# Optimization experiments

Hardware: AMD Instinct MI355X
Metric: run time of the kernel (lower is better)

The kernel has to match this reference:

```python
import jax, jax.numpy as jnp
import numpy as np

B, S, D = 4, 2048, 1024

def setup_inputs() -> dict:
    key = jax.random.key(0)
    k1, k2, k3, k4 = jax.random.split(key, 4)
    scale = 1.0 / np.sqrt(D)
    token_encodings = jax.random.normal(k1, (B, S, D), dtype=jnp.float32)
    W_q = jax.random.normal(k2, (D, D), dtype=jnp.float32) * scale
    W_k = jax.random.normal(k3, (D, D), dtype=jnp.float32) * scale
    W_v = jax.random.normal(k4, (D, D), dtype=jnp.float32) * scale
    # causal mask, broadcastable to (B, S, S); 0 means masked
    mask = jnp.tril(jnp.ones((S, S), dtype=jnp.int32))[None, :, :]
    return {"token_encodings": token_encodings, "mask": mask,
            "W_q": W_q, "W_k": W_k, "W_v": W_v}

def reference(token_encodings, mask, W_q, W_k, W_v):
    # nn.Linear(d, d, bias=False): y = x @ W.T
    q = jnp.einsum('bsd,ed->bse', token_encodings, W_q)
    k = jnp.einsum('bsd,ed->bse', token_encodings, W_k)
    v = jnp.einsum('bsd,ed->bse', token_encodings, W_v)
    d_k = q.shape[-1]
    scores = jnp.einsum('bqd,bkd->bqk', q, k) / jnp.sqrt(jnp.asarray(d_k, q.dtype))
    scores = jnp.where(mask == 0, jnp.asarray(-jnp.inf, scores.dtype), scores)
    attn_weights = jax.nn.softmax(scores, axis=-1)
    output = jnp.einsum('bqk,bkd->bqd', attn_weights, v)
    return (output, attn_weights)
```

## Files before the change

### kernel.cpp

```cpp
#include <hip/hip_runtime.h>
#include <hip/hip_bf16.h>
#include <stdint.h>
#include <math.h>


typedef __hip_bfloat16 bf16;
typedef __attribute__((ext_vector_type(8))) short short8;
typedef __attribute__((ext_vector_type(4))) float f32x4;

#define BM 128
#define BN 128
#define BK 64

static constexpr int Bb = 4;
static constexpr int S  = 2048;
static constexpr int D  = 1024;
static constexpr size_t QK_ELEMS = (size_t)Bb * S * D;
static constexpr size_t SS_ELEMS = (size_t)S * S;
static constexpr size_t W_ELEMS  = (size_t)D * D;

__device__ __forceinline__ void async16(const bf16* g, bf16* l) {
  __builtin_amdgcn_global_load_lds(
      (__attribute__((address_space(1))) const void*)g,
      (__attribute__((address_space(3))) void*)l, 16, 0, 0);
}

template<bool SWAP>
__device__ __forceinline__ void gemm_core(const bf16* __restrict__ A,
                                          const bf16* __restrict__ B,
                                          int ldA, int ldB, int ksteps,
                                          bf16* As, bf16* Bs,
                                          f32x4 acc[4][4])
{
  const int tid  = threadIdx.x;
  const int lane = tid & 63;
  const int wave = tid >> 6;
  const int wm   = (wave & 1) * 64;
  const int wn   = (wave >> 1) * 64;
  const int m16  = lane & 15;
  const int kq   = lane >> 4;
  const int sw   = m16 & 7;

  int r[4], f[4];
  #pragma unroll
  for (int i = 0; i < 4; ++i) {
    const int c = tid + i * 256;
    r[i] = c >> 3;
    f[i] = (((c & 7) ^ (r[i] & 7))) * 8;
  }

  for (int ks = 0; ks < ksteps; ++ks) {
    const int k = ks * BK;
    #pragma unroll
    for (int i = 0; i < 4; ++i)
      async16(A + (size_t)r[i] * ldA + k + f[i], As + ((size_t)tid + i * 256) * 8);
    #pragma unroll
    for (int i = 0; i < 4; ++i)
      async16(B + (size_t)r[i] * ldB + k + f[i], Bs + ((size_t)tid + i * 256) * 8);
    __syncthreads();

    #pragma unroll
    for (int j = 0; j < 2; ++j) {
      const int jc = j * 4 + kq;
      const int sl = jc ^ sw;
      short8 af[4], bfr[4];
      #pragma unroll
      for (int i = 0; i < 4; ++i)
        af[i] = *(const short8*)&As[((wm + i * 16 + m16) * 8 + sl) * 8];
      #pragma unroll
      for (int i = 0; i < 4; ++i)
        bfr[i] = *(const short8*)&Bs[((wn + i * 16 + m16) * 8 + sl) * 8];

      #pragma unroll
      for (int mi = 0; mi < 4; ++mi) {
        #pragma unroll
        for (int ni = 0; ni < 4; ++ni) {
          if (SWAP)
            acc[mi][ni] = __builtin_amdgcn_mfma_f32_16x16x32_bf16(
                bfr[ni], af[mi], acc[mi][ni], 0, 0, 0);
          else
            acc[mi][ni] = __builtin_amdgcn_mfma_f32_16x16x32_bf16(
                af[mi], bfr[ni], acc[mi][ni], 0, 0, 0);
        }
      }
    }
    __syncthreads();
  }
}

__device__ __forceinline__ void zero_acc(f32x4 acc[4][4]) {
  #pragma unroll
  for (int mi = 0; mi < 4; ++mi)
    #pragma unroll
    for (int ni = 0; ni < 4; ++ni)
      acc[mi][ni] = (f32x4){0.f, 0.f, 0.f, 0.f};
}


#define LOAD_A8(mh, ks) {                                                   \
    const bf16* ap_ = Areg + ((ks)*4 + kq)*2048 +                           \
                      (wm*128 + (mh)*64 + m16)*8;                           \
    af[0] = *(const short8*)(ap_);                                          \
    af[1] = *(const short8*)(ap_ + 128);                                    \
    af[2] = *(const short8*)(ap_ + 256);                                    \
    af[3] = *(const short8*)(ap_ + 384); }

#define LOAD_B8(ks) {                                                       \
    const bf16* bp_ = Breg + ((ks)*4 + kq)*2048 + (wn + m16)*8;             \
    bfr[0] = *(const short8*)(bp_);                                         \
    bfr[1] = *(const short8*)(bp_ + 128);                                   \
    bfr[2] = *(const short8*)(bp_ + 256);                                   \
    bfr[3] = *(const short8*)(bp_ + 384); }

#define MFMA_QUAD8(mh)                                                      \
    __builtin_amdgcn_s_setprio(1);                                          \
    _Pragma("unroll")                                                       \
    for (int mf = 0; mf < 4; ++mf) {                                        \
      _Pragma("unroll")                                                     \
      for (int nf = 0; nf < 4; ++nf) {                                      \
        if (SWAP)                                                           \
          acc[(mh)*4 + mf][nf] = __builtin_amdgcn_mfma_f32_16x16x32_bf16(   \
              bfr[nf], af[mf], acc[(mh)*4 + mf][nf], 0, 0, 0);              \
        else                                                                \
          acc[(mh)*4 + mf][nf] = __builtin_amdgcn_mfma_f32_16x16x32_bf16(   \
              af[mf], bfr[nf], acc[(mh)*4 + mf][nf], 0, 0, 0);              \
      }                                                                     \
    }                                                                       \
    __builtin_amdgcn_s_setprio(0);

template<bool SWAP>
__device__ __forceinline__ void gemm_core8(const bf16* __restrict__ A,
                                           const bf16* __restrict__ B,
                                           int ldA, int ldB, int ktiles,
                                           bf16* lds, f32x4 acc[8][4])
{
  const int tid  = threadIdx.x;
  const int lane = tid & 63;
  const int wave = tid >> 6;
  const int wm   = (wave >> 2) & 1;
  const int wn   = (wave & 3) * 64;
  const int m16  = lane & 15;
  const int kq   = lane >> 4;

  auto stage_half = [&](const bf16* Mat, int ld, int par, int matid, int ks) {
    bf16* base = lds + par * 32768 + matid * 16384 + ks * 8192;
    #pragma unroll
    for (int i = 0; i < 2; ++i) {
      const int q = tid + i * 512;
      async16(Mat + (size_t)(q & 255) * ld + ks * 32 + (q >> 8) * 8,
              base + q * 8);
    }
  };

  stage_half(A, ldA, 0, 0, 0);
  stage_half(B, ldB, 0, 1, 0);
  stage_half(A, ldA, 0, 0, 1);
  stage_half(B, ldB, 0, 1, 1);
  asm volatile("s_waitcnt vmcnt(4)" ::: "memory");
  __builtin_amdgcn_s_barrier();

  for (int t = 0; t < ktiles; ++t) {
    const int par = t & 1, npar = par ^ 1;
    const bf16* __restrict__ Areg = lds + par * 32768;
    const bf16* __restrict__ Breg = lds + par * 32768 + 16384;
    const bool pf = (t + 1 < ktiles);
    const bf16* An = A + (size_t)(t + 1) * 64;
    const bf16* Bn = B + (size_t)(t + 1) * 64;
    short8 af[4], bfr[4];

    LOAD_B8(0);
    LOAD_A8(0, 0);
    if (pf) stage_half(An, ldA, npar, 0, 0);
    __builtin_amdgcn_s_barrier();
    MFMA_QUAD8(0);
    __builtin_amdgcn_s_barrier();

    LOAD_A8(1, 0);
    if (pf) {
      stage_half(Bn, ldB, npar, 1, 0);
      asm volatile("s_waitcnt vmcnt(4)" ::: "memory");
    } else {
      asm volatile("s_waitcnt vmcnt(0)" ::: "memory");
    }
    __builtin_amdgcn_s_barrier();
    MFMA_QUAD8(1);
    __builtin_amdgcn_s_barrier();

    LOAD_B8(1);
    LOAD_A8(0, 1);
    if (pf) stage_half(An, ldA, npar, 0, 1);
    __builtin_amdgcn_s_barrier();
    MFMA_QUAD8(0);
    __builtin_amdgcn_s_barrier();

    LOAD_A8(1, 1);
    if (pf) {
      stage_half(Bn, ldB, npar, 1, 1);
      asm volatile("s_waitcnt vmcnt(4)" ::: "memory");
    } else {
      asm volatile("s_waitcnt vmcnt(0)" ::: "memory");
    }
    __builtin_amdgcn_s_barrier();
    MFMA_QUAD8(1);
    __builtin_amdgcn_s_barrier();
  }
}

__device__ __forceinline__ void zero_acc8(f32x4 acc[8][4]) {
  #pragma unroll
  for (int a = 0; a < 8; ++a)
    #pragma unroll
    for (int nf = 0; nf < 4; ++nf)
      acc[a][nf] = (f32x4){0.f, 0.f, 0.f, 0.f};
}

__device__ __forceinline__ unsigned short f2b(float f) {
  __hip_bfloat16 h = __float2bfloat16(f);
  return *(unsigned short*)&h;
}

__global__ __launch_bounds__(256)
void cvt_kernel(const float* __restrict__ X,  const float* __restrict__ Wq,
                const float* __restrict__ Wk, const float* __restrict__ Wv,
                bf16* __restrict__ Xb, bf16* __restrict__ Wqb,
                bf16* __restrict__ Wkb, bf16* __restrict__ Wvb)
{
  const size_t g = ((size_t)blockIdx.x * 256 + threadIdx.x) * 4;
  const float* src; bf16* dst; size_t off;
  if (g < QK_ELEMS) { src = X; dst = Xb; off = g; }
  else {
    const size_t h = g - QK_ELEMS;
    const int w = (int)(h >> 20);
    off = h & (W_ELEMS - 1);
    src = (w == 0) ? Wq : (w == 1) ? Wk : Wv;
    dst = (w == 0) ? Wqb : (w == 1) ? Wkb : Wvb;
  }
  const float4 v = *(const float4*)(src + off);
  uint2 o;
  o.x = (uint32_t)f2b(v.x) | ((uint32_t)f2b(v.y) << 16);
  o.y = (uint32_t)f2b(v.z) | ((uint32_t)f2b(v.w) << 16);
  *(uint2*)((unsigned short*)dst + off) = o;
}

__global__ __launch_bounds__(512, 2)
void qkv_kernel(const bf16* __restrict__ X, const bf16* __restrict__ Wq,
                const bf16* __restrict__ Wk, const bf16* __restrict__ Wv,
                bf16* __restrict__ Q, bf16* __restrict__ Ko,
                bf16* __restrict__ Vt)
{
  __shared__ __align__(16) bf16 lds[65536];
  const int L   = blockIdx.x;
  const int xcd = L & 7;
  const int i   = L >> 3;
  const int mt  = xcd * 4 + i / 12;
  const int rr_ = i % 12;
  const int z   = rr_ >> 2;
  const int nt  = rr_ & 3;
  const bf16* W = (z == 0) ? Wq : (z == 1) ? Wk : Wv;

  const int tid = threadIdx.x;
  const int lane = tid & 63, wave = tid >> 6;
  const int wm = (wave >> 2) & 1, wn = (wave & 3) * 64;
  const int col0 = lane & 15, row0 = (lane >> 4) * 4;

  f32x4 acc[8][4];
  zero_acc8(acc);
  if (z < 2) {
    gemm_core8<false>(X + (size_t)mt * 256 * D, W + (size_t)nt * 256 * D,
                      D, D, D / 64, lds, acc);
    bf16* Out = z ? Ko : Q;
    #pragma unroll
    for (int a = 0; a < 8; ++a)
      #pragma unroll
      for (int nf = 0; nf < 4; ++nf)
        #pragma unroll
        for (int r = 0; r < 4; ++r) {
          const int grow = mt * 256 + wm * 128 + a * 16 + row0 + r;
          const int gcol = nt * 256 + wn + nf * 16 + col0;
          Out[(size_t)grow * D + gcol] = __float2bfloat16(acc[a][nf][r]);
        }
  } else {
    gemm_core8<true>(X + (size_t)mt * 256 * D, W + (size_t)nt * 256 * D,
                     D, D, D / 64, lds, acc);
    const int b = mt >> 3;
    #pragma unroll
    for (int a = 0; a < 8; ++a)
      #pragma unroll
      for (int nf = 0; nf < 4; ++nf)
        #pragma unroll
        for (int r = 0; r < 4; ++r) {
          const int ge = nt * 256 + wn + nf * 16 + row0 + r;
          const int gs = mt * 256 + wm * 128 + a * 16 + col0;
          const int sl = gs & (S - 1);
          Vt[(size_t)b * D * S + (size_t)ge * S + sl] = __float2bfloat16(acc[a][nf][r]);
        }
  }
}

__global__ __launch_bounds__(512, 2)
void scores_kernel(const bf16* __restrict__ Q, const bf16* __restrict__ K,
                   float* __restrict__ Sc)
{
  const int t = blockIdx.x, b = blockIdx.y;
  int qt = (int)((sqrtf(8.f * (float)t + 1.f) - 1.f) * 0.5f);
  while ((qt + 1) * (qt + 2) / 2 <= t) ++qt;
  while (qt * (qt + 1) / 2 > t) --qt;
  const int kt = t - qt * (qt + 1) / 2;

  __shared__ __align__(16) bf16 lds[65536];

  f32x4 acc[8][4];
  zero_acc8(acc);
  gemm_core8<false>(Q + ((size_t)b * S + qt * 256) * D,
                    K + ((size_t)b * S + kt * 256) * D,
                    D, D, D / 64, lds, acc);

  const int tid = threadIdx.x;
  const int lane = tid & 63, wave = tid >> 6;
  const int wm = (wave >> 2) & 1, wn = (wave & 3) * 64;
  const int col0 = lane & 15, row0 = (lane >> 4) * 4;
  float* out = Sc + (size_t)b * SS_ELEMS;
  #pragma unroll
  for (int a = 0; a < 8; ++a)
    #pragma unroll
    for (int nf = 0; nf < 4; ++nf)
      #pragma unroll
      for (int r = 0; r < 4; ++r) {
        const int gq = qt * 256 + wm * 128 + a * 16 + row0 + r;
        const int gk = kt * 256 + wn + nf * 16 + col0;
        out[(size_t)gq * S + gk] = acc[a][nf][r] * 0.03125f;
      }
}

__device__ __forceinline__ float wave_max(float v) {
  #pragma unroll
  for (int o = 32; o > 0; o >>= 1) v = fmaxf(v, __shfl_xor(v, o, 64));
  return v;
}
__device__ __forceinline__ float wave_sum(float v) {
  #pragma unroll
  for (int o = 32; o > 0; o >>= 1) v += __shfl_xor(v, o, 64);
  return v;
}

__global__ __launch_bounds__(256)
void softmax_kernel(float* __restrict__ Attn, bf16* __restrict__ Pb)
{
  const int row = blockIdx.x;
  const int b = row >> 11, i = row & (S - 1);
  float* s = Attn + (size_t)b * SS_ELEMS + (size_t)i * S;
  bf16* p  = Pb   + (size_t)b * SS_ELEMS + (size_t)i * S;
  const int t = threadIdx.x;
  const int lane = t & 63, wave = t >> 6;
  __shared__ float red[4];

  float4 v[2];
  #pragma unroll
  for (int u = 0; u < 2; ++u) {
    const int base = (t + u * 256) * 4;
    if (base + 3 <= i) {
      v[u] = *(const float4*)(s + base);
    } else if (base > i) {
      v[u] = make_float4(-INFINITY, -INFINITY, -INFINITY, -INFINITY);
    } else {
      v[u].x = (base + 0 <= i) ? s[base + 0] : -INFINITY;
      v[u].y = (base + 1 <= i) ? s[base + 1] : -INFINITY;
      v[u].z = (base + 2 <= i) ? s[base + 2] : -INFINITY;
      v[u].w = (base + 3 <= i) ? s[base + 3] : -INFINITY;
    }
  }

  float m = -INFINITY;
  #pragma unroll
  for (int u = 0; u < 2; ++u)
    m = fmaxf(m, fmaxf(fmaxf(v[u].x, v[u].y), fmaxf(v[u].z, v[u].w)));
  m = wave_max(m);
  if (lane == 0) red[wave] = m;
  __syncthreads();
  m = fmaxf(fmaxf(red[0], red[1]), fmaxf(red[2], red[3]));
  __syncthreads();

  float sum = 0.f;
  #pragma unroll
  for (int u = 0; u < 2; ++u) {
    v[u].x = expf(v[u].x - m); sum += v[u].x;
    v[u].y = expf(v[u].y - m); sum += v[u].y;
    v[u].z = expf(v[u].z - m); sum += v[u].z;
    v[u].w = expf(v[u].w - m); sum += v[u].w;
  }
  sum = wave_sum(sum);
  if (lane == 0) red[wave] = sum;
  __syncthreads();
  sum = red[0] + red[1] + red[2] + red[3];
  const float inv = 1.f / sum;

  const int dt_end = ((i >> 7) + 1) * 128;
  #pragma unroll
  for (int u = 0; u < 2; ++u) {
    const int base = (t + u * 256) * 4;
    float4 w;
    w.x = v[u].x * inv; w.y = v[u].y * inv;
    w.z = v[u].z * inv; w.w = v[u].w * inv;
    *(float4*)(s + base) = w;
    if (base < dt_end) {
      ushort4 pk;
      pk.x = f2b(w.x); pk.y = f2b(w.y); pk.z = f2b(w.z); pk.w = f2b(w.w);
      *(ushort4*)((unsigned short*)p + base) = pk;
    }
  }
}

__global__ __launch_bounds__(256, 4)
void out_kernel(const bf16* __restrict__ P, const bf16* __restrict__ Vt,
                float* __restrict__ O)
{
  const int L = blockIdx.x;
  const int x = L & 7;
  const int s = L >> 3;
  const int dt  = s & 7;
  const int qtb = ((s >> 3) << 3) | x;
  const int qt  = 15 - (qtb >> 2);
  const int b   = qtb & 3;

  __shared__ __align__(16) bf16 As[BM * BK];
  __shared__ __align__(16) bf16 Bs[BN * BK];

  f32x4 acc[4][4];
  zero_acc(acc);
  const int ksteps = (qt + 1) * (128 / BK);
  gemm_core<false>(P + (size_t)b * SS_ELEMS + (size_t)qt * 128 * S,
                   Vt + (size_t)b * D * S + (size_t)dt * 128 * S,
                   S, S, ksteps, As, Bs, acc);

  const int lane = threadIdx.x & 63, wave = threadIdx.x >> 6;
  const int wm = (wave & 1) * 64, wn = (wave >> 1) * 64;
  const int col0 = lane & 15, row0 = (lane >> 4) * 4;
  #pragma unroll
  for (int mi = 0; mi < 4; ++mi)
    #pragma unroll
    for (int ni = 0; ni < 4; ++ni)
      #pragma unroll
      for (int r = 0; r < 4; ++r) {
        const int gq = qt * 128 + wm + mi * 16 + row0 + r;
        const int gd = dt * 128 + wn + ni * 16 + col0;
        O[((size_t)b * S + gq) * D + gd] = acc[mi][ni][r];
      }
}

extern "C" void kernel_launch(void* const* d_in, const int* in_sizes, int n_in,
                              void* d_out, int out_size, void* d_ws, size_t ws_size,
                              hipStream_t stream) {
  const float* X  = (const float*)d_in[0];
  const float* Wq = (const float*)d_in[2];
  const float* Wk = (const float*)d_in[3];
  const float* Wv = (const float*)d_in[4];

  float* Out  = (float*)d_out;
  float* Attn = Out + QK_ELEMS;

  bf16* Q   = (bf16*)d_ws;
  bf16* K   = Q + QK_ELEMS;
  bf16* Vt  = K + QK_ELEMS;
  bf16* Xb  = Vt + QK_ELEMS;
  bf16* Wqb = Xb + QK_ELEMS;
  bf16* Wkb = Wqb + W_ELEMS;
  bf16* Wvb = Wkb + W_ELEMS;
  bf16* Pb  = (bf16*)d_ws;

  const int cvt_blocks = (int)((QK_ELEMS + 3 * W_ELEMS) / 4 / 256);
  cvt_kernel<<<cvt_blocks, 256, 0, stream>>>(X, Wq, Wk, Wv, Xb, Wqb, Wkb, Wvb);
  qkv_kernel<<<dim3(384), 512, 0, stream>>>(Xb, Wqb, Wkb, Wvb, Q, K, Vt);
  const int ntile = (S / 256) * (S / 256 + 1) / 2;
  scores_kernel<<<dim3(ntile, Bb), 512, 0, stream>>>(Q, K, Attn);
  softmax_kernel<<<dim3(Bb * S), 256, 0, stream>>>(Attn, Pb);
  out_kernel<<<dim3(512), 256, 0, stream>>>(Pb, Vt, Out);
}
```

Before: 319.3 us.

## Deepen GEMM prefetch pipeline with early-staged halves and peeled tail iterations

Reworks the GEMM main loop so that global-to-LDS loads are issued roughly two k-tiles ahead. Buffer halves are reused as soon as their fragments have been read, and the last two iterations are peeled out so the loop needs no per-step prefetch conditionals. Separately, the QKV block-index mapping is reordered so that blocks for the same projection (Q/K/V) are grouped together, changing L2 reuse patterns of weights and inputs. The intent is to hide more memory latency. In exchange, the schedule relies on precise vmcnt counts and careful buffer-reuse ordering, which risks races if any wait count is wrong.

```diff
diff --git a/kernel.cpp b/kernel.cpp
--- a/kernel.cpp
+++ b/kernel.cpp
@@ -152,57 +152,116 @@
     }
   };
 
-  stage_half(A, ldA, 0, 0, 0);
-  stage_half(B, ldB, 0, 1, 0);
-  stage_half(A, ldA, 0, 0, 1);
-  stage_half(B, ldB, 0, 1, 1);
-  asm volatile("s_waitcnt vmcnt(4)" ::: "memory");
+  stage_half(A,      ldA, 0, 0, 0);
+  stage_half(B,      ldB, 0, 1, 0);
+  stage_half(A,      ldA, 0, 0, 1);
+  stage_half(B,      ldB, 0, 1, 1);
+  stage_half(A + 64, ldA, 1, 0, 0);
+  stage_half(B + 64, ldB, 1, 1, 0);
+  stage_half(B + 64, ldB, 1, 1, 1);
+  asm volatile("s_waitcnt vmcnt(10)" ::: "memory");
   __builtin_amdgcn_s_barrier();
 
-  for (int t = 0; t < ktiles; ++t) {
+  for (int t = 0; t + 2 < ktiles; ++t) {
     const int par = t & 1, npar = par ^ 1;
     const bf16* __restrict__ Areg = lds + par * 32768;
-    const bf16* __restrict__ Breg = lds + par * 32768 + 16384;
-    const bool pf = (t + 1 < ktiles);
-    const bf16* An = A + (size_t)(t + 1) * 64;
-    const bf16* Bn = B + (size_t)(t + 1) * 64;
+    const bf16* __restrict__ Breg = Areg + 16384;
+    const bf16* A1 = A + (size_t)(t + 1) * 64;
+    const bf16* A2 = A + (size_t)(t + 2) * 64;
+    const bf16* B2 = B + (size_t)(t + 2) * 64;
     short8 af[4], bfr[4];
 
     LOAD_B8(0);
     LOAD_A8(0, 0);
-    if (pf) stage_half(An, ldA, npar, 0, 0);
+    stage_half(A1, ldA, npar, 0, 1);
     __builtin_amdgcn_s_barrier();
     MFMA_QUAD8(0);
     __builtin_amdgcn_s_barrier();
 
     LOAD_A8(1, 0);
-    if (pf) {
-      stage_half(Bn, ldB, npar, 1, 0);
-      asm volatile("s_waitcnt vmcnt(4)" ::: "memory");
-    } else {
-      asm volatile("s_waitcnt vmcnt(0)" ::: "memory");
-    }
+    stage_half(B2, ldB, par, 1, 0);
+    asm volatile("s_waitcnt vmcnt(10)" ::: "memory");
     __builtin_amdgcn_s_barrier();
     MFMA_QUAD8(1);
     __builtin_amdgcn_s_barrier();
 
     LOAD_B8(1);
     LOAD_A8(0, 1);
-    if (pf) stage_half(An, ldA, npar, 0, 1);
+    stage_half(A2, ldA, par, 0, 0);
     __builtin_amdgcn_s_barrier();
     MFMA_QUAD8(0);
     __builtin_amdgcn_s_barrier();
 
     LOAD_A8(1, 1);
-    if (pf) {
-      stage_half(Bn, ldB, npar, 1, 1);
-      asm volatile("s_waitcnt vmcnt(4)" ::: "memory");
-    } else {
-      asm volatile("s_waitcnt vmcnt(0)" ::: "memory");
-    }
+    stage_half(B2, ldB, par, 1, 1);
+    asm volatile("s_waitcnt vmcnt(10)" ::: "memory");
     __builtin_amdgcn_s_barrier();
     MFMA_QUAD8(1);
     __builtin_amdgcn_s_barrier();
+  }
+
+  {
+    const int t = ktiles - 2;
+    const int par = t & 1, npar = par ^ 1;
+    const bf16* __restrict__ Areg = lds + par * 32768;
+    const bf16* __restrict__ Breg = Areg + 16384;
+    const bf16* A1 = A + (size_t)(t + 1) * 64;
+    short8 af[4], bfr[4];
+
+    LOAD_B8(0);
+    LOAD_A8(0, 0);
+    stage_half(A1, ldA, npar, 0, 1);
+    __builtin_amdgcn_s_barrier();
+    MFMA_QUAD8(0);
+    __builtin_amdgcn_s_barrier();
+
+    LOAD_A8(1, 0);
+    asm volatile("s_waitcnt vmcnt(8)" ::: "memory");
+    __builtin_amdgcn_s_barrier();
+    MFMA_QUAD8(1);
+    __builtin_amdgcn_s_barrier();
+
+    LOAD_B8(1);
+    LOAD_A8(0, 1);
+    __builtin_amdgcn_s_barrier();
+    MFMA_QUAD8(0);
+    __builtin_amdgcn_s_barrier();
+
+    LOAD_A8(1, 1);
+    asm volatile("s_waitcnt vmcnt(4)" ::: "memory");
+    __builtin_amdgcn_s_barrier();
+    MFMA_QUAD8(1);
+    __builtin_amdgcn_s_barrier();
+  }
+
+  {
+    const int t = ktiles - 1;
+    const int par = t & 1;
+    const bf16* __restrict__ Areg = lds + par * 32768;
+    const bf16* __restrict__ Breg = Areg + 16384;
+    short8 af[4], bfr[4];
+
+    LOAD_B8(0);
+    LOAD_A8(0, 0);
+    __builtin_amdgcn_s_barrier();
+    MFMA_QUAD8(0);
+    __builtin_amdgcn_s_barrier();
+
+    LOAD_A8(1, 0);
+    asm volatile("s_waitcnt vmcnt(0)" ::: "memory");
+    __builtin_amdgcn_s_barrier();
+    MFMA_QUAD8(1);
+    __builtin_amdgcn_s_barrier();
+
+    LOAD_B8(1);
+    LOAD_A8(0, 1);
+    __builtin_amdgcn_s_barrier();
+    MFMA_QUAD8(0);
+    __builtin_amdgcn_s_barrier();
+
+    LOAD_A8(1, 1);
+    __builtin_amdgcn_s_barrier();
+    MFMA_QUAD8(1);
   }
 }
 
@@ -251,11 +310,11 @@
   __shared__ __align__(16) bf16 lds[65536];
   const int L   = blockIdx.x;
   const int xcd = L & 7;
-  const int i   = L >> 3;
-  const int mt  = xcd * 4 + i / 12;
-  const int rr_ = i % 12;
-  const int z   = rr_ >> 2;
-  const int nt  = rr_ & 3;
+  const int G   = L >> 3;
+  const int z   = G >> 4;
+  const int r_  = G & 15;
+  const int mt  = xcd * 4 + (r_ >> 2);
+  const int nt  = r_ & 3;
   const bf16* W = (z == 0) ? Wq : (z == 1) ? Wk : Wv;
 
   const int tid = threadIdx.x;
```

Measured after the change: 326.1 us. 2.1% more time.
